# Optimization experiments

Measured on AMD Instinct MI355X. Metric: run time of the kernel, lower is better.

## Reference

```python
import jax, jax.numpy as jnp
import numpy as np

SCALE = 4.0  # VeRA scale hyperparameter


def setup_inputs() -> dict:
    key = jax.random.key(0)
    ks = jax.random.split(key, 7)
    T, IN, OUT, R = 8192, 4096, 4096, 256
    return {
        "x": jax.random.normal(ks[0], (T, IN), dtype=jnp.float32),
        "base_weight": jax.random.normal(ks[1], (OUT, IN), dtype=jnp.float32) * 0.02,
        "base_bias": jax.random.normal(ks[2], (OUT,), dtype=jnp.float32) * 0.02,
        "vera_random_A": jax.random.normal(ks[3], (R, IN), dtype=jnp.float32) * (1.0 / np.sqrt(IN)),
        "vera_random_B": jax.random.normal(ks[4], (OUT, R), dtype=jnp.float32) * (1.0 / np.sqrt(R)),
        "vera_d": jax.random.normal(ks[5], (R,), dtype=jnp.float32) * 0.01,
        "vera_b": 0.1 * jnp.ones((OUT,), dtype=jnp.float32),
    }


def reference(x, base_weight, base_bias, vera_random_A, vera_random_B, vera_d, vera_b):
    # delta_W = scale * diag(vera_b) @ B @ diag(vera_d) @ A  -> row/col scaling, no diag matmuls
    # shapes: B (out, r), A (r, in), delta (out, in)
    delta = SCALE * jnp.einsum("or,ri->oi", vera_b[:, None] * vera_random_B, vera_d[:, None] * vera_random_A)
    # linear: y = x @ (W + delta)^T + bias
    return x @ (base_weight + delta).T + base_bias
```

## Files before the change

kernel.cpp:

```cpp
#include <hip/hip_runtime.h>


typedef __attribute__((ext_vector_type(8))) short short8;
typedef __attribute__((ext_vector_type(4))) float f32x4;

__device__ __forceinline__ unsigned short f2bf(float f) {
  union { float f; unsigned int u; } c; c.f = f;
  unsigned int u = c.u;
  unsigned int r = (u + 0x7fffu + ((u >> 16) & 1u)) >> 16;
  return (unsigned short)r;
}

__device__ __forceinline__ void gl2lds16(const unsigned short* g, unsigned short* l) {
  __builtin_amdgcn_global_load_lds(
      (const __attribute__((address_space(1))) unsigned int*)g,
      (__attribute__((address_space(3))) unsigned int*)l, 16, 0, 0);
}

__global__ __launch_bounds__(256) void k_pre(const float* __restrict__ x,
                                             unsigned short* __restrict__ xb,
                                             const float* __restrict__ Bv,
                                             const float* __restrict__ Av,
                                             const float* __restrict__ dv,
                                             const float* __restrict__ bv,
                                             unsigned short* __restrict__ Bd,
                                             unsigned short* __restrict__ AbT) {
  __shared__ float tl[32][33];
  const int blk = blockIdx.x;
  const int tid = threadIdx.x;
  if (blk < 8192) {
#pragma unroll
    for (int s = 0; s < 4; ++s) {
      int i = blk * 1024 + s * 256 + tid;
      const float4 v = ((const float4*)x)[i];
      union { unsigned short u[4]; unsigned long long ll; } o;
      o.u[0] = f2bf(v.x); o.u[1] = f2bf(v.y); o.u[2] = f2bf(v.z); o.u[3] = f2bf(v.w);
      ((unsigned long long*)xb)[i] = o.ll;
    }
  } else if (blk < 12288) {
    int idx = (blk - 8192) * 256 + tid;
    int o = idx >> 8, r = idx & 255;
    Bd[idx] = f2bf(4.0f * bv[o] * Bv[idx] * dv[r]);
  } else {
    int blk2 = blk - 12288;
    int ti = blk2 >> 3;
    int tr = blk2 & 7;
#pragma unroll
    for (int s = 0; s < 4; ++s) {
      int r = tr * 32 + s * 8 + (tid >> 5);
      int i = ti * 32 + (tid & 31);
      tl[s * 8 + (tid >> 5)][tid & 31] = Av[(size_t)r * 4096 + i];
    }
    __syncthreads();
#pragma unroll
    for (int s = 0; s < 4; ++s) {
      int iloc = s * 8 + (tid >> 5);
      int rloc = tid & 31;
      AbT[(size_t)(ti * 32 + iloc) * 256 + tr * 32 + rloc] = f2bf(tl[rloc][iloc]);
    }
  }
}

template <int FOLD>
__global__ __launch_bounds__(256) void gemm_bt(const unsigned short* __restrict__ Amat,
                                               const unsigned short* __restrict__ Bmat,
                                               int K, int N,
                                               const float* __restrict__ extra,
                                               float* __restrict__ outF,
                                               unsigned short* __restrict__ outB) {
  __shared__ unsigned short As[128 * 64];
  __shared__ unsigned short Bs[128 * 64];

  const int tid  = threadIdx.x;
  const int lane = tid & 63;
  const int wave = tid >> 6;
  const int wm   = wave >> 1;
  const int wn   = wave & 1;
  const int quad = lane >> 4;
  const int m16  = lane & 15;
  const int s7   = m16 & 7;

  const int blockN = blockIdx.x * 128;
  const int blockM = blockIdx.y * 128;

  const int c    = tid & 7;
  const int rsub = tid >> 3;

  size_t aOff[4], bOff[4];
  unsigned short *dA[4], *dB[4];
#pragma unroll
  for (int n = 0; n < 4; ++n) {
    const int r = n * 32 + rsub;
    const int src = (c ^ (r & 7)) * 8;
    aOff[n] = (size_t)(blockM + r) * K + src;
    bOff[n] = (size_t)(blockN + r) * K + src;
    dA[n] = &As[(size_t)n * 2048 + tid * 8];
    dB[n] = &Bs[(size_t)n * 2048 + tid * 8];
  }

  f32x4 acc[4][4];
#pragma unroll
  for (int i = 0; i < 4; ++i)
#pragma unroll
    for (int j = 0; j < 4; ++j) acc[i][j] = (f32x4){0.f, 0.f, 0.f, 0.f};

  const short8* Asv = (const short8*)As;
  const short8* Bsv = (const short8*)Bs;

  for (int k0 = 0; k0 < K; k0 += 64) {
    __syncthreads();
#pragma unroll
    for (int n = 0; n < 4; ++n) {
      gl2lds16(Amat + aOff[n] + k0, dA[n]);
      gl2lds16(Bmat + bOff[n] + k0, dB[n]);
    }
    __syncthreads();

#pragma unroll
    for (int h = 0; h < 2; ++h) {
      const int qs = (h * 4 + quad) ^ s7;
      short8 af[4], bf[4];
#pragma unroll
      for (int t = 0; t < 4; ++t) {
        af[t] = Asv[(wm * 64 + t * 16 + m16) * 8 + qs];
        bf[t] = Bsv[(wn * 64 + t * 16 + m16) * 8 + qs];
      }
#pragma unroll
      for (int mt = 0; mt < 4; ++mt)
#pragma unroll
        for (int nt = 0; nt < 4; ++nt)
          acc[mt][nt] = __builtin_amdgcn_mfma_f32_16x16x32_bf16(af[mt], bf[nt], acc[mt][nt], 0, 0, 0);
    }
  }

#pragma unroll
  for (int mt = 0; mt < 4; ++mt) {
    const int row0 = blockM + wm * 64 + mt * 16 + quad * 4;
#pragma unroll
    for (int nt = 0; nt < 4; ++nt) {
      const int col = blockN + wn * 64 + nt * 16 + m16;
      f32x4 v = acc[mt][nt];
      if (FOLD) {
#pragma unroll
        for (int r = 0; r < 4; ++r) {
          size_t o = (size_t)(row0 + r) * N + col;
          outB[o] = f2bf(extra[o] + v[r]);
        }
      } else {
        const float bv = extra[col];
#pragma unroll
        for (int r = 0; r < 4; ++r) {
          size_t o = (size_t)(row0 + r) * N + col;
          outF[o] = v[r] + bv;
        }
      }
    }
  }
}

extern "C" void kernel_launch(void* const* d_in, const int* in_sizes, int n_in,
                              void* d_out, int out_size, void* d_ws, size_t ws_size,
                              hipStream_t stream) {
  const float* x    = (const float*)d_in[0];
  const float* W    = (const float*)d_in[1];
  const float* bias = (const float*)d_in[2];
  const float* A    = (const float*)d_in[3];
  const float* B    = (const float*)d_in[4];
  const float* dv   = (const float*)d_in[5];
  const float* bv   = (const float*)d_in[6];
  float* out = (float*)d_out;

  char* ws = (char*)d_ws;
  unsigned short* xb  = (unsigned short*)ws;
  unsigned short* Wc  = (unsigned short*)(ws + (size_t)(64 << 20));
  unsigned short* Bd  = (unsigned short*)(ws + (size_t)(96 << 20));
  unsigned short* AbT = (unsigned short*)(ws + (size_t)(98 << 20));

  hipLaunchKernelGGL(k_pre, dim3(13312), dim3(256), 0, stream,
                     x, xb, B, A, dv, bv, Bd, AbT);
  hipLaunchKernelGGL((gemm_bt<1>), dim3(32, 32), dim3(256), 0, stream,
                     Bd, AbT, 256, 4096, W, (float*)nullptr, Wc);
  hipLaunchKernelGGL((gemm_bt<0>), dim3(32, 64), dim3(256), 0, stream,
                     xb, Wc, 4096, 4096, bias, out, (unsigned short*)nullptr);
}
```

Baseline: 589.6 us.

## Rewrite GEMM with 256x256 tiles, double-buffered async LDS loads, and XCD-aware block mapping

Replaces the 128x128 single-buffered GEMM with a 512-thread 256x256 tile kernel. The K loop is split into half-tiles, and global-to-LDS loads for later k-steps are issued while MFMAs run on the current buffer, using explicit vmcnt waits and raw barriers. It also adds a workgroup remap that spreads blocks across the eight XCDs, plus MFMA priority hints. The goal is more data reuse per tile and hiding load latency. The cost is a larger register footprint from 32 accumulators per thread and hand-tuned wait counts that must match the issue order.

```diff
diff --git a/kernel.cpp b/kernel.cpp
--- a/kernel.cpp
+++ b/kernel.cpp
@@ -62,80 +62,125 @@
 }
 
 template <int FOLD>
-__global__ __launch_bounds__(256) void gemm_bt(const unsigned short* __restrict__ Amat,
-                                               const unsigned short* __restrict__ Bmat,
-                                               int K, int N,
-                                               const float* __restrict__ extra,
-                                               float* __restrict__ outF,
-                                               unsigned short* __restrict__ outB) {
-  __shared__ unsigned short As[128 * 64];
-  __shared__ unsigned short Bs[128 * 64];
+__global__ __launch_bounds__(512, 2) void gemm256(const unsigned short* __restrict__ Amat,
+                                                  const unsigned short* __restrict__ Bmat,
+                                                  int K, int N, int NBY,
+                                                  const float* __restrict__ extra,
+                                                  float* __restrict__ outF,
+                                                  unsigned short* __restrict__ outB) {
+  __shared__ __align__(16) unsigned short As[2 * 2 * 8192];
+  __shared__ __align__(16) unsigned short Bs[2 * 2 * 8192];
 
   const int tid  = threadIdx.x;
   const int lane = tid & 63;
   const int wave = tid >> 6;
-  const int wm   = wave >> 1;
-  const int wn   = wave & 1;
+  const int wm   = wave >> 2;
+  const int wn   = wave & 3;
   const int quad = lane >> 4;
   const int m16  = lane & 15;
-  const int s7   = m16 & 7;
-
-  const int blockN = blockIdx.x * 128;
-  const int blockM = blockIdx.y * 128;
-
-  const int c    = tid & 7;
-  const int rsub = tid >> 3;
-
-  size_t aOff[4], bOff[4];
-  unsigned short *dA[4], *dB[4];
-#pragma unroll
-  for (int n = 0; n < 4; ++n) {
-    const int r = n * 32 + rsub;
-    const int src = (c ^ (r & 7)) * 8;
-    aOff[n] = (size_t)(blockM + r) * K + src;
-    bOff[n] = (size_t)(blockN + r) * K + src;
-    dA[n] = &As[(size_t)n * 2048 + tid * 8];
-    dB[n] = &Bs[(size_t)n * 2048 + tid * 8];
-  }
-
-  f32x4 acc[4][4];
-#pragma unroll
-  for (int i = 0; i < 4; ++i)
-#pragma unroll
-    for (int j = 0; j < 4; ++j) acc[i][j] = (f32x4){0.f, 0.f, 0.f, 0.f};
+  const int qsl  = quad ^ ((m16 >> 1) & 3);
+
+  const int nwg  = gridDim.x;
+  const int cpx  = nwg >> 3;
+  const int wgid = (blockIdx.x & 7) * cpx + (blockIdx.x >> 3);
+  const int by   = wgid % NBY;
+  const int bx   = wgid / NBY;
+  const int blockM = by * 256;
+  const int blockN = bx * 256;
+
+  const int srow = tid >> 2;
+  const int sq8  = ((tid & 3) ^ ((tid >> 3) & 3)) * 8;
+  const size_t aB0 = (size_t)(blockM + srow) * K + sq8;
+  const size_t aB1 = aB0 + (size_t)128 * K;
+  const size_t bB0 = (size_t)(blockN + srow) * K + sq8;
+  const size_t bB1 = bB0 + (size_t)128 * K;
 
   const short8* Asv = (const short8*)As;
   const short8* Bsv = (const short8*)Bs;
-
-  for (int k0 = 0; k0 < K; k0 += 64) {
-    __syncthreads();
-#pragma unroll
-    for (int n = 0; n < 4; ++n) {
-      gl2lds16(Amat + aOff[n] + k0, dA[n]);
-      gl2lds16(Bmat + bOff[n] + k0, dB[n]);
-    }
-    __syncthreads();
-
-#pragma unroll
-    for (int h = 0; h < 2; ++h) {
-      const int qs = (h * 4 + quad) ^ s7;
-      short8 af[4], bf[4];
-#pragma unroll
-      for (int t = 0; t < 4; ++t) {
-        af[t] = Asv[(wm * 64 + t * 16 + m16) * 8 + qs];
-        bf[t] = Bsv[(wn * 64 + t * 16 + m16) * 8 + qs];
-      }
-#pragma unroll
-      for (int mt = 0; mt < 4; ++mt)
-#pragma unroll
-        for (int nt = 0; nt < 4; ++nt)
-          acc[mt][nt] = __builtin_amdgcn_mfma_f32_16x16x32_bf16(af[mt], bf[nt], acc[mt][nt], 0, 0, 0);
-    }
+  const int aRd = wm * 512 + m16 * 4 + qsl;
+  const int bRd = wn * 256 + m16 * 4 + qsl;
+
+  f32x4 acc[8][4];
+#pragma unroll
+  for (int i = 0; i < 8; ++i)
+#pragma unroll
+    for (int j = 0; j < 4; ++j) acc[i][j] = (f32x4){0.f, 0.f, 0.f, 0.f};
+
+  short8 afr[4], bfr[4];
+
+#define WAITV(n) asm volatile("s_waitcnt vmcnt(" #n ") lgkmcnt(0)" ::: "memory")
+
+#define ISSUE_A(bufi, kh, koff) do {                                         \
+    unsigned short* d_ = As + ((bufi) * 2 + (kh)) * 8192 + tid * 8;          \
+    gl2lds16(Amat + aB0 + (koff) + (kh) * 32, d_);                           \
+    gl2lds16(Amat + aB1 + (koff) + (kh) * 32, d_ + 4096);                    \
+  } while (0)
+
+#define ISSUE_B(bufi, kh, koff) do {                                         \
+    unsigned short* d_ = Bs + ((bufi) * 2 + (kh)) * 8192 + tid * 8;          \
+    gl2lds16(Bmat + bB0 + (koff) + (kh) * 32, d_);                           \
+    gl2lds16(Bmat + bB1 + (koff) + (kh) * 32, d_ + 4096);                    \
+  } while (0)
+
+#define RD_B(Bb, h) do {                                                     \
+    _Pragma("unroll") for (int nt = 0; nt < 4; ++nt)                         \
+      bfr[nt] = Bsv[((Bb) * 2 + (h)) * 1024 + bRd + nt * 64];                \
+  } while (0)
+
+#define RD_A(Bb, h, mh) do {                                                 \
+    _Pragma("unroll") for (int mt = 0; mt < 4; ++mt)                         \
+      afr[mt] = Asv[((Bb) * 2 + (h)) * 1024 + aRd + (mh) * 256 + mt * 64];   \
+  } while (0)
+
+#define MM(mh) do {                                                          \
+    __builtin_amdgcn_s_setprio(1);                                           \
+    _Pragma("unroll") for (int mt = 0; mt < 4; ++mt)                         \
+    _Pragma("unroll") for (int nt = 0; nt < 4; ++nt)                         \
+      acc[(mh) * 4 + mt][nt] = __builtin_amdgcn_mfma_f32_16x16x32_bf16(      \
+          afr[mt], bfr[nt], acc[(mh) * 4 + mt][nt], 0, 0, 0);                \
+    __builtin_amdgcn_s_setprio(0);                                           \
+  } while (0)
+
+#define TILE(Bb, ko, W1, W3, I12, I34) do {                                  \
+    WAITV(W1);                                                               \
+    __builtin_amdgcn_s_barrier();                                            \
+    if (I12) ISSUE_A((Bb) ^ 1, 1, (ko) + 64);                                \
+    RD_B(Bb, 0); RD_A(Bb, 0, 0); MM(0);                                      \
+    if (I12) ISSUE_B((Bb) ^ 1, 1, (ko) + 64);                                \
+    RD_A(Bb, 0, 1); MM(1);                                                   \
+    WAITV(W3);                                                               \
+    __builtin_amdgcn_s_barrier();                                            \
+    if (I34) ISSUE_A(Bb, 0, (ko) + 128);                                     \
+    RD_B(Bb, 1); RD_A(Bb, 1, 0); MM(0);                                      \
+    if (I34) ISSUE_B(Bb, 0, (ko) + 128);                                     \
+    RD_A(Bb, 1, 1); MM(1);                                                   \
+  } while (0)
+
+  ISSUE_A(0, 0, (size_t)0);  ISSUE_B(0, 0, (size_t)0);
+  ISSUE_A(0, 1, (size_t)0);  ISSUE_B(0, 1, (size_t)0);
+  ISSUE_A(1, 0, (size_t)64); ISSUE_B(1, 0, (size_t)64);
+
+  const int NT = K >> 6;
+  size_t ko = 0;
+  for (int t = 0; t < NT - 2; t += 2) {
+    TILE(0, ko, 8, 8, 1, 1);
+    TILE(1, ko + 64, 8, 8, 1, 1);
+    ko += 128;
   }
-
-#pragma unroll
-  for (int mt = 0; mt < 4; ++mt) {
-    const int row0 = blockM + wm * 64 + mt * 16 + quad * 4;
+  TILE(0, ko, 8, 8, 1, 0);
+  TILE(1, ko + 64, 4, 0, 0, 0);
+
+#undef WAITV
+#undef ISSUE_A
+#undef ISSUE_B
+#undef RD_B
+#undef RD_A
+#undef MM
+#undef TILE
+
+#pragma unroll
+  for (int mt = 0; mt < 8; ++mt) {
+    const int row0 = blockM + wm * 128 + mt * 16 + quad * 4;
 #pragma unroll
     for (int nt = 0; nt < 4; ++nt) {
       const int col = blockN + wn * 64 + nt * 16 + m16;
@@ -147,11 +192,11 @@
           outB[o] = f2bf(extra[o] + v[r]);
         }
       } else {
-        const float bv = extra[col];
+        const float bb = extra[col];
 #pragma unroll
         for (int r = 0; r < 4; ++r) {
           size_t o = (size_t)(row0 + r) * N + col;
-          outF[o] = v[r] + bv;
+          outF[o] = v[r] + bb;
         }
       }
     }
@@ -178,8 +223,8 @@
 
   hipLaunchKernelGGL(k_pre, dim3(13312), dim3(256), 0, stream,
                      x, xb, B, A, dv, bv, Bd, AbT);
-  hipLaunchKernelGGL((gemm_bt<1>), dim3(32, 32), dim3(256), 0, stream,
-                     Bd, AbT, 256, 4096, W, (float*)nullptr, Wc);
-  hipLaunchKernelGGL((gemm_bt<0>), dim3(32, 64), dim3(256), 0, stream,
-                     xb, Wc, 4096, 4096, bias, out, (unsigned short*)nullptr);
-}
+  hipLaunchKernelGGL((gemm256<1>), dim3(256), dim3(512), 0, stream,
+                     Bd, AbT, 256, 4096, 16, W, (float*)nullptr, Wc);
+  hipLaunchKernelGGL((gemm256<0>), dim3(512), dim3(512), 0, stream,
+                     xb, Wc, 4096, 4096, 32, bias, out, (unsigned short*)nullptr);
+}
```

Measured after the change: 547.5 us. -7.1%, faster.
